# Kernel tuning notes

Hardware: AMD Instinct MI355X
Metric: run time of the kernel (lower is better)

## Reference

```python
import jax, jax.numpy as jnp
import numpy as np

NUM_USERS = 100000
NUM_ITEMS = 50000
EMB = 64
K = 3
NUM_EDGES = 1250000
N = NUM_USERS + NUM_ITEMS


def setup_inputs() -> dict:
    key = jax.random.key(0)
    k1, k2, k3 = jax.random.split(key, 3)
    edge_index = jax.random.randint(k1, (2, NUM_EDGES), 0, N, dtype=jnp.int64)
    # Xavier-uniform-like init for embedding tables
    bound = float(np.sqrt(6.0 / (N + EMB)))
    user_weight = jax.random.uniform(k2, (NUM_USERS, EMB), jnp.float32, -bound, bound)
    item_weight = jax.random.uniform(k3, (NUM_ITEMS, EMB), jnp.float32, -bound, bound)
    return {"user_weight": user_weight, "item_weight": item_weight, "edge_index": edge_index}


def reference(user_weight, item_weight, edge_index):
    src = edge_index[0]
    dst = edge_index[1]
    # PyG gcn_norm with add_self_loops=False: deg over destination (col),
    # norm = deg^{-1/2}[src] * deg^{-1/2}[dst], isolated nodes -> 0.
    ones = jnp.ones((src.shape[0],), jnp.float32)
    deg = jax.ops.segment_sum(ones, dst, num_segments=N)
    dis = jnp.where(deg > 0, jax.lax.rsqrt(jnp.maximum(deg, 1.0)), 0.0)
    norm = dis[src] * dis[dst]  # [E]

    x = jnp.concatenate([user_weight, item_weight], axis=0)  # [N, D]
    out = x
    for _ in range(K):
        # LGConv: x' = sum_{(s->d)} norm * x[s]
        msg = x[src] * norm[:, None]  # [E, D]
        x = jax.ops.segment_sum(msg, dst, num_segments=N)
        out = out + x
    out = out / (K + 1)
    return out[:NUM_USERS], out[NUM_USERS:]
```

## Files before the change

### kernel.cpp

```cpp
#include <hip/hip_runtime.h>

#define NUM_USERS 100000
#define NUM_ITEMS 50000
#define EMB 64
#define NUM_EDGES 1250000
#define NNODES (NUM_USERS + NUM_ITEMS)
#define NELEM (NNODES * EMB)
#define SCAN_CHUNK 1024
#define NBLK_SCAN ((NNODES + SCAN_CHUNK - 1) / SCAN_CHUNK)

__global__ void hist_rank_c(const int4* __restrict__ dst4, int* __restrict__ counts,
                            int4* __restrict__ rank4) {
    int i = blockIdx.x * blockDim.x + threadIdx.x;
    if (i < NUM_EDGES / 4) {
        int4 d = dst4[i];
        int4 r;
        r.x = atomicAdd(&counts[d.x], 1);
        r.y = atomicAdd(&counts[d.y], 1);
        r.z = atomicAdd(&counts[d.z], 1);
        r.w = atomicAdd(&counts[d.w], 1);
        rank4[i] = r;
    }
}

__global__ void scan1_c(const int* __restrict__ counts, int* __restrict__ blksum) {
    __shared__ int lds[256];
    int base = blockIdx.x * SCAN_CHUNK;
    int t = threadIdx.x;
    int s = 0;
#pragma unroll
    for (int j = 0; j < 4; ++j) {
        int i = base + t * 4 + j;
        if (i < NNODES) s += counts[i];
    }
    lds[t] = s;
    __syncthreads();
    for (int off = 128; off > 0; off >>= 1) {
        if (t < off) lds[t] += lds[t + off];
        __syncthreads();
    }
    if (t == 0) blksum[blockIdx.x] = lds[0];
}

__global__ void scan2_c(int* __restrict__ blksum) {
    __shared__ int lds[256];
    int t = threadIdx.x;
    int v = (t < NBLK_SCAN) ? blksum[t] : 0;
    lds[t] = v;
    __syncthreads();
    for (int off = 1; off < 256; off <<= 1) {
        int add = (t >= off) ? lds[t - off] : 0;
        __syncthreads();
        lds[t] += add;
        __syncthreads();
    }
    if (t < NBLK_SCAN) blksum[t] = lds[t] - v;
}

__global__ void scan3_c(const int* __restrict__ counts, const int* __restrict__ blksum,
                        int* __restrict__ offs, float* __restrict__ dis,
                        float* __restrict__ invdeg, float* __restrict__ rdis) {
    __shared__ int lds[256];
    int base = blockIdx.x * SCAN_CHUNK;
    int t = threadIdx.x;
    int c[4];
    int s = 0;
#pragma unroll
    for (int j = 0; j < 4; ++j) {
        int i = base + t * 4 + j;
        c[j] = (i < NNODES) ? counts[i] : 0;
        s += c[j];
    }
    lds[t] = s;
    __syncthreads();
    for (int off = 1; off < 256; off <<= 1) {
        int add = (t >= off) ? lds[t - off] : 0;
        __syncthreads();
        lds[t] += add;
        __syncthreads();
    }
    int run = blksum[blockIdx.x] + lds[t] - s;
#pragma unroll
    for (int j = 0; j < 4; ++j) {
        int i = base + t * 4 + j;
        if (i < NNODES) {
            float fc = (float)c[j];
            offs[i]   = run;
            dis[i]    = (c[j] > 0) ? (1.0f / sqrtf(fc)) : 0.0f;
            invdeg[i] = (c[j] > 0) ? (1.0f / fc) : 0.0f;
            rdis[i]   = (c[j] > 0) ? sqrtf(fc) : 0.0f;
            run += c[j];
        }
    }
}

__global__ void scatter_c(const int4* __restrict__ src4, const int4* __restrict__ dst4,
                          const int4* __restrict__ rank4, const int* __restrict__ offs,
                          int* __restrict__ entries) {
    int i = blockIdx.x * blockDim.x + threadIdx.x;
    if (i < NUM_EDGES / 4) {
        int4 s = src4[i];
        int4 d = dst4[i];
        int4 r = rank4[i];
        entries[offs[d.x] + r.x] = s.x;
        entries[offs[d.y] + r.y] = s.y;
        entries[offs[d.z] + r.z] = s.z;
        entries[offs[d.w] + r.w] = s.w;
    }
}

__global__ void y0_c(const float4* __restrict__ uw4, const float4* __restrict__ iw4,
                     const float* __restrict__ dis, float4* __restrict__ y0) {
    int i = blockIdx.x * blockDim.x + threadIdx.x;
    const int nuser4 = NUM_USERS * EMB / 4;
    if (i < NELEM / 4) {
        float4 v = (i < nuser4) ? uw4[i] : iw4[i - nuser4];
        float w = dis[i >> 4];
        v.x *= w; v.y *= w; v.z *= w; v.w *= w;
        y0[i] = v;
    }
}

__device__ __forceinline__ void gacc_c(float4& a, const float4* __restrict__ y,
                                       int s, int chunk) {
    float4 v = y[((size_t)s << 4) + chunk];
    a.x += v.x; a.y += v.y; a.z += v.z; a.w += v.w;
}

template <bool FINAL>
__global__ __launch_bounds__(256)
void pull_c(const int* __restrict__ entries, const int* __restrict__ offs,
            const int* __restrict__ deg, const float* __restrict__ invdeg,
            const float4* __restrict__ yin,
            const float* __restrict__ dis, const float* __restrict__ rdis,
            const float4* __restrict__ y1,
            const float* __restrict__ uw, const float* __restrict__ iw,
            float4* __restrict__ out) {
    int gid  = blockIdx.x * blockDim.x + threadIdx.x;
    int n    = gid >> 6;
    if (n >= NNODES) return;
    int lane  = gid & 63;
    int grp   = lane >> 4;
    int chunk = lane & 15;

    const int* ebase = entries + offs[n];
    int dg = deg[n];

    float4 a0 = {0,0,0,0}, a1 = {0,0,0,0}, a2 = {0,0,0,0}, a3 = {0,0,0,0};

    for (int base = 0; base < dg; base += 64) {
        int rem = dg - base; if (rem > 64) rem = 64;
        int ent = 0;
        if (lane < rem) ent = ebase[base + lane];
        for (int it = 0; it < rem; it += 16) {
            int p = it + grp;
            int s0 = __shfl(ent, p);
            int s1 = __shfl(ent, p + 4);
            int s2 = __shfl(ent, p + 8);
            int s3 = __shfl(ent, p + 12);
            if (p      < rem) gacc_c(a0, yin, s0, chunk);
            if (p + 4  < rem) gacc_c(a1, yin, s1, chunk);
            if (p + 8  < rem) gacc_c(a2, yin, s2, chunk);
            if (p + 12 < rem) gacc_c(a3, yin, s3, chunk);
        }
    }

    float4 a;
    a.x = (a0.x + a1.x) + (a2.x + a3.x);
    a.y = (a0.y + a1.y) + (a2.y + a3.y);
    a.z = (a0.z + a1.z) + (a2.z + a3.z);
    a.w = (a0.w + a1.w) + (a2.w + a3.w);
    a.x += __shfl_xor(a.x, 16); a.y += __shfl_xor(a.y, 16);
    a.z += __shfl_xor(a.z, 16); a.w += __shfl_xor(a.w, 16);
    a.x += __shfl_xor(a.x, 32); a.y += __shfl_xor(a.y, 32);
    a.z += __shfl_xor(a.z, 32); a.w += __shfl_xor(a.w, 32);

    if (lane < 16) {
        size_t ro = ((size_t)n << 4) + chunk;
        if (FINAL) {
            const float* xrow = (n < NUM_USERS) ? uw + ((size_t)n << 6)
                                                : iw + ((size_t)(n - NUM_USERS) << 6);
            float4 x0v = *(const float4*)(xrow + (chunk << 2));
            float4 b = y1[ro];
            float4 c = yin[ro];
            float rd = rdis[n], di = dis[n];
            float4 o;
            o.x = 0.25f * (x0v.x + rd * (b.x + c.x) + di * a.x);
            o.y = 0.25f * (x0v.y + rd * (b.y + c.y) + di * a.y);
            o.z = 0.25f * (x0v.z + rd * (b.z + c.z) + di * a.z);
            o.w = 0.25f * (x0v.w + rd * (b.w + c.w) + di * a.w);
            out[ro] = o;
        } else {
            float iv = invdeg[n];
            a.x *= iv; a.y *= iv; a.z *= iv; a.w *= iv;
            out[ro] = a;
        }
    }
}

extern "C" void kernel_launch(void* const* d_in, const int* in_sizes, int n_in,
                              void* d_out, int out_size, void* d_ws, size_t ws_size,
                              hipStream_t stream) {
    const float* uw  = (const float*)d_in[0];
    const float* iw  = (const float*)d_in[1];
    const int*   ei  = (const int*)d_in[2];
    const int*   src = ei;
    const int*   dst = ei + NUM_EDGES;

    float* out = (float*)d_out;

    char*  ws      = (char*)d_ws;
    float* y1      = (float*)ws;
    float* y2      = y1 + NELEM;
    int*   entries = (int*)(y2 + NELEM);
    int*   counts  = entries + NUM_EDGES;
    int*   offs    = counts + NNODES;
    float* dis     = (float*)(offs + NNODES);
    float* invdeg  = dis + NNODES;
    float* rdis    = invdeg + NNODES;
    int*   blksum  = (int*)(rdis + NNODES);
    int*   rank    = (int*)y1;

    const int B = 256;
    const int eblk = (NUM_EDGES / 4 + B - 1) / B;

    hipMemsetAsync(counts, 0, NNODES * sizeof(int), stream);
    hist_rank_c<<<eblk, B, 0, stream>>>((const int4*)dst, counts, (int4*)rank);
    scan1_c<<<NBLK_SCAN, B, 0, stream>>>(counts, blksum);
    scan2_c<<<1, B, 0, stream>>>(blksum);
    scan3_c<<<NBLK_SCAN, B, 0, stream>>>(counts, blksum, offs, dis, invdeg, rdis);
    scatter_c<<<eblk, B, 0, stream>>>((const int4*)src, (const int4*)dst,
                                      (const int4*)rank, offs, entries);

    y0_c<<<(NELEM / 4 + B - 1) / B, B, 0, stream>>>(
        (const float4*)uw, (const float4*)iw, dis, (float4*)out);

    const int pull_blocks = (NNODES * 64) / B;
    pull_c<false><<<pull_blocks, B, 0, stream>>>(
        entries, offs, counts, invdeg, (const float4*)out, dis, rdis,
        nullptr, nullptr, nullptr, (float4*)y1);
    pull_c<false><<<pull_blocks, B, 0, stream>>>(
        entries, offs, counts, invdeg, (const float4*)y1, dis, rdis,
        nullptr, nullptr, nullptr, (float4*)y2);
    pull_c<true><<<pull_blocks, B, 0, stream>>>(
        entries, offs, counts, invdeg, (const float4*)y2, dis, rdis,
        (const float4*)y1, uw, iw, (float4*)out);
}
```

Baseline: 375.4 us.

## Map one node per 16 lanes in pull kernels and fuse y0 scaling into first pull

The pull kernels now give each node 16 lanes (one float4 chunk per lane) instead of a full 64-lane wave. Each thread walks the node's neighbour list sequentially, unrolled by four, so the cross-group shuffle reduction goes away. The separate y0 kernel is removed: the first pull reads the raw embeddings and scales each by dis[src] on the fly, saving one full pass over the embeddings. In exchange, each node's neighbours are loaded serially and the first pull performs an extra dis gather per edge; high-degree nodes may also cause load imbalance within a wave.

```diff
diff --git a/kernel.cpp b/kernel.cpp
--- a/kernel.cpp
+++ b/kernel.cpp
@@ -9,7 +9,7 @@
 #define SCAN_CHUNK 1024
 #define NBLK_SCAN ((NNODES + SCAN_CHUNK - 1) / SCAN_CHUNK)
 
-__global__ void hist_rank_c(const int4* __restrict__ dst4, int* __restrict__ counts,
+__global__ void hist_rank_d(const int4* __restrict__ dst4, int* __restrict__ counts,
                             int4* __restrict__ rank4) {
     int i = blockIdx.x * blockDim.x + threadIdx.x;
     if (i < NUM_EDGES / 4) {
@@ -23,7 +23,7 @@
     }
 }
 
-__global__ void scan1_c(const int* __restrict__ counts, int* __restrict__ blksum) {
+__global__ void scan1_d(const int* __restrict__ counts, int* __restrict__ blksum) {
     __shared__ int lds[256];
     int base = blockIdx.x * SCAN_CHUNK;
     int t = threadIdx.x;
@@ -42,7 +42,7 @@
     if (t == 0) blksum[blockIdx.x] = lds[0];
 }
 
-__global__ void scan2_c(int* __restrict__ blksum) {
+__global__ void scan2_d(int* __restrict__ blksum) {
     __shared__ int lds[256];
     int t = threadIdx.x;
     int v = (t < NBLK_SCAN) ? blksum[t] : 0;
@@ -57,7 +57,7 @@
     if (t < NBLK_SCAN) blksum[t] = lds[t] - v;
 }
 
-__global__ void scan3_c(const int* __restrict__ counts, const int* __restrict__ blksum,
+__global__ void scan3_d(const int* __restrict__ counts, const int* __restrict__ blksum,
                         int* __restrict__ offs, float* __restrict__ dis,
                         float* __restrict__ invdeg, float* __restrict__ rdis) {
     __shared__ int lds[256];
@@ -94,7 +94,7 @@
     }
 }
 
-__global__ void scatter_c(const int4* __restrict__ src4, const int4* __restrict__ dst4,
+__global__ void scatter_d(const int4* __restrict__ src4, const int4* __restrict__ dst4,
                           const int4* __restrict__ rank4, const int* __restrict__ offs,
                           int* __restrict__ entries) {
     int i = blockIdx.x * blockDim.x + threadIdx.x;
@@ -109,60 +109,61 @@
     }
 }
 
-__global__ void y0_c(const float4* __restrict__ uw4, const float4* __restrict__ iw4,
-                     const float* __restrict__ dis, float4* __restrict__ y0) {
-    int i = blockIdx.x * blockDim.x + threadIdx.x;
-    const int nuser4 = NUM_USERS * EMB / 4;
-    if (i < NELEM / 4) {
-        float4 v = (i < nuser4) ? uw4[i] : iw4[i - nuser4];
-        float w = dis[i >> 4];
-        v.x *= w; v.y *= w; v.z *= w; v.w *= w;
-        y0[i] = v;
-    }
-}
-
-__device__ __forceinline__ void gacc_c(float4& a, const float4* __restrict__ y,
-                                       int s, int chunk) {
-    float4 v = y[((size_t)s << 4) + chunk];
+__device__ __forceinline__ void gaccy_d(float4& a, const float4* __restrict__ y,
+                                        int s, int c) {
+    float4 v = y[((size_t)s << 4) + c];
     a.x += v.x; a.y += v.y; a.z += v.z; a.w += v.w;
 }
 
-template <bool FINAL>
+__device__ __forceinline__ void gacc0_d(float4& a, const float* __restrict__ uw,
+                                        const float* __restrict__ iw,
+                                        const float* __restrict__ dis, int s, int c) {
+    float w = dis[s];
+    const float* xr = (s < NUM_USERS) ? (uw + ((size_t)s << 6))
+                                      : (iw + ((size_t)(s - NUM_USERS) << 6));
+    float4 v = *(const float4*)(xr + (c << 2));
+    a.x = fmaf(w, v.x, a.x); a.y = fmaf(w, v.y, a.y);
+    a.z = fmaf(w, v.z, a.z); a.w = fmaf(w, v.w, a.w);
+}
+
+template <int MODE>
 __global__ __launch_bounds__(256)
-void pull_c(const int* __restrict__ entries, const int* __restrict__ offs,
+void pull_d(const int* __restrict__ entries, const int* __restrict__ offs,
             const int* __restrict__ deg, const float* __restrict__ invdeg,
             const float4* __restrict__ yin,
             const float* __restrict__ dis, const float* __restrict__ rdis,
             const float4* __restrict__ y1,
             const float* __restrict__ uw, const float* __restrict__ iw,
             float4* __restrict__ out) {
-    int gid  = blockIdx.x * blockDim.x + threadIdx.x;
-    int n    = gid >> 6;
+    int gid = blockIdx.x * blockDim.x + threadIdx.x;
+    int n   = gid >> 4;
     if (n >= NNODES) return;
-    int lane  = gid & 63;
-    int grp   = lane >> 4;
-    int chunk = lane & 15;
-
-    const int* ebase = entries + offs[n];
+    int c   = gid & 15;
+
+    const int* eb = entries + offs[n];
     int dg = deg[n];
 
     float4 a0 = {0,0,0,0}, a1 = {0,0,0,0}, a2 = {0,0,0,0}, a3 = {0,0,0,0};
 
-    for (int base = 0; base < dg; base += 64) {
-        int rem = dg - base; if (rem > 64) rem = 64;
-        int ent = 0;
-        if (lane < rem) ent = ebase[base + lane];
-        for (int it = 0; it < rem; it += 16) {
-            int p = it + grp;
-            int s0 = __shfl(ent, p);
-            int s1 = __shfl(ent, p + 4);
-            int s2 = __shfl(ent, p + 8);
-            int s3 = __shfl(ent, p + 12);
-            if (p      < rem) gacc_c(a0, yin, s0, chunk);
-            if (p + 4  < rem) gacc_c(a1, yin, s1, chunk);
-            if (p + 8  < rem) gacc_c(a2, yin, s2, chunk);
-            if (p + 12 < rem) gacc_c(a3, yin, s3, chunk);
+    int j = 0;
+    for (; j + 4 <= dg; j += 4) {
+        int s0 = eb[j], s1 = eb[j + 1], s2 = eb[j + 2], s3 = eb[j + 3];
+        if (MODE == 0) {
+            gacc0_d(a0, uw, iw, dis, s0, c);
+            gacc0_d(a1, uw, iw, dis, s1, c);
+            gacc0_d(a2, uw, iw, dis, s2, c);
+            gacc0_d(a3, uw, iw, dis, s3, c);
+        } else {
+            gaccy_d(a0, yin, s0, c);
+            gaccy_d(a1, yin, s1, c);
+            gaccy_d(a2, yin, s2, c);
+            gaccy_d(a3, yin, s3, c);
         }
+    }
+    for (; j < dg; ++j) {
+        int s0 = eb[j];
+        if (MODE == 0) gacc0_d(a0, uw, iw, dis, s0, c);
+        else           gaccy_d(a0, yin, s0, c);
     }
 
     float4 a;
@@ -170,31 +171,25 @@
     a.y = (a0.y + a1.y) + (a2.y + a3.y);
     a.z = (a0.z + a1.z) + (a2.z + a3.z);
     a.w = (a0.w + a1.w) + (a2.w + a3.w);
-    a.x += __shfl_xor(a.x, 16); a.y += __shfl_xor(a.y, 16);
-    a.z += __shfl_xor(a.z, 16); a.w += __shfl_xor(a.w, 16);
-    a.x += __shfl_xor(a.x, 32); a.y += __shfl_xor(a.y, 32);
-    a.z += __shfl_xor(a.z, 32); a.w += __shfl_xor(a.w, 32);
-
-    if (lane < 16) {
-        size_t ro = ((size_t)n << 4) + chunk;
-        if (FINAL) {
-            const float* xrow = (n < NUM_USERS) ? uw + ((size_t)n << 6)
-                                                : iw + ((size_t)(n - NUM_USERS) << 6);
-            float4 x0v = *(const float4*)(xrow + (chunk << 2));
-            float4 b = y1[ro];
-            float4 c = yin[ro];
-            float rd = rdis[n], di = dis[n];
-            float4 o;
-            o.x = 0.25f * (x0v.x + rd * (b.x + c.x) + di * a.x);
-            o.y = 0.25f * (x0v.y + rd * (b.y + c.y) + di * a.y);
-            o.z = 0.25f * (x0v.z + rd * (b.z + c.z) + di * a.z);
-            o.w = 0.25f * (x0v.w + rd * (b.w + c.w) + di * a.w);
-            out[ro] = o;
-        } else {
-            float iv = invdeg[n];
-            a.x *= iv; a.y *= iv; a.z *= iv; a.w *= iv;
-            out[ro] = a;
-        }
+
+    size_t ro = ((size_t)n << 4) + c;
+    if (MODE == 2) {
+        const float* xrow = (n < NUM_USERS) ? uw + ((size_t)n << 6)
+                                            : iw + ((size_t)(n - NUM_USERS) << 6);
+        float4 x0v = *(const float4*)(xrow + (c << 2));
+        float4 b = y1[ro];
+        float4 d2 = yin[ro];
+        float rd = rdis[n], di = dis[n];
+        float4 o;
+        o.x = 0.25f * (x0v.x + rd * (b.x + d2.x) + di * a.x);
+        o.y = 0.25f * (x0v.y + rd * (b.y + d2.y) + di * a.y);
+        o.z = 0.25f * (x0v.z + rd * (b.z + d2.z) + di * a.z);
+        o.w = 0.25f * (x0v.w + rd * (b.w + d2.w) + di * a.w);
+        out[ro] = o;
+    } else {
+        float iv = invdeg[n];
+        a.x *= iv; a.y *= iv; a.z *= iv; a.w *= iv;
+        out[ro] = a;
     }
 }
 
@@ -225,24 +220,21 @@
     const int eblk = (NUM_EDGES / 4 + B - 1) / B;
 
     hipMemsetAsync(counts, 0, NNODES * sizeof(int), stream);
-    hist_rank_c<<<eblk, B, 0, stream>>>((const int4*)dst, counts, (int4*)rank);
-    scan1_c<<<NBLK_SCAN, B, 0, stream>>>(counts, blksum);
-    scan2_c<<<1, B, 0, stream>>>(blksum);
-    scan3_c<<<NBLK_SCAN, B, 0, stream>>>(counts, blksum, offs, dis, invdeg, rdis);
-    scatter_c<<<eblk, B, 0, stream>>>((const int4*)src, (const int4*)dst,
+    hist_rank_d<<<eblk, B, 0, stream>>>((const int4*)dst, counts, (int4*)rank);
+    scan1_d<<<NBLK_SCAN, B, 0, stream>>>(counts, blksum);
+    scan2_d<<<1, B, 0, stream>>>(blksum);
+    scan3_d<<<NBLK_SCAN, B, 0, stream>>>(counts, blksum, offs, dis, invdeg, rdis);
+    scatter_d<<<eblk, B, 0, stream>>>((const int4*)src, (const int4*)dst,
                                       (const int4*)rank, offs, entries);
 
-    y0_c<<<(NELEM / 4 + B - 1) / B, B, 0, stream>>>(
-        (const float4*)uw, (const float4*)iw, dis, (float4*)out);
-
-    const int pull_blocks = (NNODES * 64) / B;
-    pull_c<false><<<pull_blocks, B, 0, stream>>>(
-        entries, offs, counts, invdeg, (const float4*)out, dis, rdis,
-        nullptr, nullptr, nullptr, (float4*)y1);
-    pull_c<false><<<pull_blocks, B, 0, stream>>>(
+    const int pull_blocks = (NNODES * 16 + B - 1) / B;
+    pull_d<0><<<pull_blocks, B, 0, stream>>>(
+        entries, offs, counts, invdeg, nullptr, dis, nullptr,
+        nullptr, uw, iw, (float4*)y1);
+    pull_d<1><<<pull_blocks, B, 0, stream>>>(
         entries, offs, counts, invdeg, (const float4*)y1, dis, rdis,
         nullptr, nullptr, nullptr, (float4*)y2);
-    pull_c<true><<<pull_blocks, B, 0, stream>>>(
+    pull_d<2><<<pull_blocks, B, 0, stream>>>(
         entries, offs, counts, invdeg, (const float4*)y2, dis, rdis,
         (const float4*)y1, uw, iw, (float4*)out);
 }
```

Result: faster. 327.6 us (-12.7%).
